# Kernel tuning notes

Hardware: AMD Instinct MI355X
Metric: run time of the kernel (lower is better)

Reference implementation:

```python
import jax, jax.numpy as jnp
import numpy as np

N, C, H, W = 4, 256, 64, 64
D = 128  # inter_channels = C // 2


def setup_inputs() -> dict:
    key = jax.random.key(0)
    ks = jax.random.split(key, 9)
    s = 0.05  # weight scale
    return {
        "x": jax.random.normal(ks[0], (N, C, H, W), jnp.float32),
        "Wg": jax.random.normal(ks[1], (D, C), jnp.float32) * s,
        "bg": jax.random.normal(ks[2], (D,), jnp.float32) * s,
        "Wt": jax.random.normal(ks[3], (D, C), jnp.float32) * s,
        "bt": jax.random.normal(ks[4], (D,), jnp.float32) * s,
        "Wp": jax.random.normal(ks[5], (D, C), jnp.float32) * s,
        "bp": jax.random.normal(ks[6], (D,), jnp.float32) * s,
        "Wz": jax.random.normal(ks[7], (C, D), jnp.float32) * s,
        "bz": jax.random.normal(ks[8], (C,), jnp.float32) * s,
    }


def reference(x, Wg, bg, Wt, bt, Wp, bp, Wz, bz):
    # NonLocalBlock, mode='embedded', dimension=2, bn_layer=False.
    # 1x1 convs are per-pixel linear maps over channels.
    n, c, h, w = x.shape
    xf = x.reshape(n, c, h * w)                                  # (N,C,S)
    g_x = jnp.einsum('dc,ncs->nds', Wg, xf) + bg[None, :, None]  # (N,D,S)
    th = jnp.einsum('dc,ncs->nds', Wt, xf) + bt[None, :, None]   # (N,D,S)
    ph = jnp.einsum('dc,ncs->nds', Wp, xf) + bp[None, :, None]   # (N,D,S)
    f = jnp.einsum('nds,ndt->nst', th, ph)                       # (N,S,S)
    att = jax.nn.softmax(f, axis=-1)
    y = jnp.einsum('nst,ndt->nds', att, g_x)                     # (N,D,S)
    w_y = jnp.einsum('cd,nds->ncs', Wz, y) + bz[None, :, None]   # (N,C,S)
    return (w_y + xf).reshape(n, c, h, w)
```

## Files before the change

### kernel.cpp

```cpp
#include <hip/hip_runtime.h>
#include <math.h>

#define N_ 4
#define C_ 256
#define D_ 128
#define S_ 4096
#define LOG2E 1.4426950408889634f
#define SPLIT 4
#define TPS 16

typedef __attribute__((ext_vector_type(4))) float f32x4;
typedef __attribute__((ext_vector_type(16))) float f32x16;
typedef __attribute__((ext_vector_type(8))) short short8;
typedef __attribute__((ext_vector_type(8))) unsigned short ushort8;
typedef __attribute__((ext_vector_type(4))) unsigned short ushort4v;

#define MFMA16(a, b, c) __builtin_amdgcn_mfma_f32_16x16x32_bf16((a), (b), (c), 0, 0, 0)
#define MFMA32(a, b, c) __builtin_amdgcn_mfma_f32_32x32x16_bf16((a), (b), (c), 0, 0, 0)

__device__ __forceinline__ unsigned short f2bf(float f) {
  union { float f; unsigned int u; } v; v.f = f;
  unsigned int r = v.u + 0x7fffu + ((v.u >> 16) & 1u);
  return (unsigned short)(r >> 16);
}
__device__ __forceinline__ float bf2f(unsigned short u) {
  union { unsigned int u; float f; } v; v.u = ((unsigned int)u) << 16;
  return v.f;
}
__device__ __forceinline__ unsigned cvtpk(float lo, float hi) {
  unsigned r;
  asm("v_cvt_pk_bf16_f32 %0, %1, %2" : "=v"(r) : "v"(lo), "v"(hi));
  return r;
}
__device__ __forceinline__ float vmax16(const f32x16& v) {
  float a = fmaxf(fmaxf(v[0], v[1]), fmaxf(v[2], v[3]));
  float b = fmaxf(fmaxf(v[4], v[5]), fmaxf(v[6], v[7]));
  float c = fmaxf(fmaxf(v[8], v[9]), fmaxf(v[10], v[11]));
  float d = fmaxf(fmaxf(v[12], v[13]), fmaxf(v[14], v[15]));
  return fmaxf(fmaxf(a, b), fmaxf(c, d));
}
__device__ __forceinline__ float vsum16(const f32x16& v) {
  float a = (v[0] + v[1]) + (v[2] + v[3]);
  float b = (v[4] + v[5]) + (v[6] + v[7]);
  float c = (v[8] + v[9]) + (v[10] + v[11]);
  float d = (v[12] + v[13]) + (v[14] + v[15]);
  return (a + b) + (c + d);
}
__device__ __forceinline__ void gload16(const void* g, void* l) {
  __builtin_amdgcn_global_load_lds((const __attribute__((address_space(1))) unsigned int*)g,
                                   (__attribute__((address_space(3))) unsigned int*)l,
                                   16, 0, 0);
}

__global__ void k_convw(const float* __restrict__ w0, const float* __restrict__ w1,
                        const float* __restrict__ w2, const float* __restrict__ w3,
                        unsigned short* __restrict__ d0, unsigned short* __restrict__ d1,
                        unsigned short* __restrict__ d2, unsigned short* __restrict__ d3) {
  int b = blockIdx.x;
  int w = b >> 4;
  int i = (b & 15) * 256 + threadIdx.x;
  const float* s = (w == 0) ? w0 : (w == 1) ? w1 : (w == 2) ? w2 : w3;
  unsigned short* d = (w == 0) ? d0 : (w == 1) ? d1 : (w == 2) ? d2 : d3;
  const float4* sp = reinterpret_cast<const float4*>(s) + (size_t)i * 2;
  float4 a = sp[0], c = sp[1];
  ushort8 o;
  o[0] = f2bf(a.x); o[1] = f2bf(a.y); o[2] = f2bf(a.z); o[3] = f2bf(a.w);
  o[4] = f2bf(c.x); o[5] = f2bf(c.y); o[6] = f2bf(c.z); o[7] = f2bf(c.w);
  reinterpret_cast<ushort8*>(d)[i] = o;
}

__global__ __launch_bounds__(256, 2) void k_proj(
    const float* __restrict__ x,
    const unsigned short* __restrict__ wg, const unsigned short* __restrict__ wt,
    const unsigned short* __restrict__ wp,
    const float* __restrict__ bg, const float* __restrict__ bt, const float* __restrict__ bp,
    unsigned short* __restrict__ qb, unsigned short* __restrict__ kb, unsigned short* __restrict__ vb)
{
  __shared__ __align__(16) unsigned short xs[C_ * 64];
  const int tid = threadIdx.x;
  const int n = blockIdx.x >> 6;
  const int s0 = (blockIdx.x & 63) << 6;
  const float* xsrc = x + (size_t)n * C_ * S_ + s0;
#pragma unroll
  for (int i = 0; i < 16; ++i) {
    int ch = i * 256 + tid;
    int c = ch >> 4, s4 = (ch & 15) << 2;
    float4 v = *reinterpret_cast<const float4*>(xsrc + (size_t)c * S_ + s4);
    ushort4v o;
    o[0] = f2bf(v.x); o[1] = f2bf(v.y); o[2] = f2bf(v.z); o[3] = f2bf(v.w);
    *reinterpret_cast<ushort4v*>(xs + c * 64 + s4) = o;
  }
  __syncthreads();
  const int lane = tid & 63, wid = tid >> 6;
  const int l15 = lane & 15, g = lane >> 4;
  const int scol = wid * 16 + l15;

  short8 bx[8];
#pragma unroll
  for (int kc = 0; kc < 8; ++kc) {
    int cb = kc * 32 + g * 8;
    short8 t;
#pragma unroll
    for (int j = 0; j < 8; ++j) t[j] = (short)xs[(cb + j) * 64 + scol];
    bx[kc] = t;
  }

  const f32x4 fz = {0.f, 0.f, 0.f, 0.f};
  for (int p = 0; p < 3; ++p) {
    const unsigned short* W = (p == 0) ? wg : ((p == 1) ? wt : wp);
    const float* bias = (p == 0) ? bg : ((p == 1) ? bt : bp);
    f32x4 acc[8];
#pragma unroll
    for (int dt = 0; dt < 8; ++dt) acc[dt] = fz;
#pragma unroll
    for (int dt = 0; dt < 8; ++dt) {
      const unsigned short* wrow = W + (size_t)(dt * 16 + l15) * C_ + g * 8;
#pragma unroll
      for (int kc = 0; kc < 8; ++kc) {
        short8 a = *reinterpret_cast<const short8*>(wrow + kc * 32);
        acc[dt] = MFMA16(a, bx[kc], acc[dt]);
      }
    }
    if (p == 0) {
#pragma unroll
      for (int dt = 0; dt < 8; ++dt) {
#pragma unroll
        for (int r = 0; r < 4; ++r) {
          int d = dt * 16 + 4 * g + r;
          vb[((size_t)n * D_ + d) * S_ + s0 + scol] = f2bf(acc[dt][r] + bias[d]);
        }
      }
    } else {
      unsigned short* dst = (p == 1) ? qb : kb;
      unsigned short* row = dst + ((size_t)(n * S_) + s0 + scol) * D_;
#pragma unroll
      for (int dt = 0; dt < 8; ++dt) {
        ushort4v o;
#pragma unroll
        for (int r = 0; r < 4; ++r) o[r] = f2bf(acc[dt][r] + bias[dt * 16 + 4 * g + r]);
        *reinterpret_cast<ushort4v*>(row + dt * 16 + 4 * g) = o;
      }
    }
  }
}

__global__ __launch_bounds__(256, 2) void k_attn(
    const unsigned short* __restrict__ qb, const unsigned short* __restrict__ kb,
    const unsigned short* __restrict__ vb,
    unsigned short* __restrict__ opart, float2* __restrict__ ml)
{
  __shared__ __align__(16) unsigned short ksm[2][64 * 128];
  __shared__ __align__(16) unsigned short vsm[2][128 * 64];
  const int tid = threadIdx.x, lane = tid & 63, w = tid >> 6;
  const int l31 = lane & 31, hi = lane >> 5;
  const int b = blockIdx.x;
  const int sp = b & 3, qt = (b >> 2) & 31, n = b >> 7;
  const int q0 = qt << 7;

  unsigned koff[4], voff[4], ubo[4];
#pragma unroll
  for (int j = 0; j < 4; ++j) {
    int f = j * 256 + tid;
    int kr = f >> 4, kc = f & 15;
    koff[j] = kr * D_ + ((kc ^ (kr & 7)) << 3);
    int vr = f >> 3, vc = f & 7;
    voff[j] = vr * S_ + ((vc ^ (vr & 7)) << 3);
    ubo[j] = (unsigned)(j * 256 + (tid & 192)) * 8;
  }
  const unsigned short* kb0 = kb + ((size_t)n * S_ + (size_t)sp * TPS * 64) * D_;
  const unsigned short* vb0 = vb + (size_t)n * D_ * S_ + sp * TPS * 64;

  auto stage = [&](int buf, int t) {
    const unsigned short* kt = kb0 + (size_t)t * 64 * D_;
    const unsigned short* vt = vb0 + t * 64;
#pragma unroll
    for (int j = 0; j < 4; ++j) gload16(kt + koff[j], &ksm[buf][ubo[j]]);
#pragma unroll
    for (int j = 0; j < 4; ++j) gload16(vt + voff[j], &vsm[buf][ubo[j]]);
  };

  stage(0, 0);

  const unsigned short* qsrc = qb + ((size_t)(n * S_) + q0 + w * 32 + l31) * D_;
  short8 qf[8];
#pragma unroll
  for (int k = 0; k < 8; ++k)
    qf[k] = *reinterpret_cast<const short8*>(qsrc + k * 16 + hi * 8);

  const f32x16 z16 = {0.f,0.f,0.f,0.f,0.f,0.f,0.f,0.f,0.f,0.f,0.f,0.f,0.f,0.f,0.f,0.f};
  f32x16 oacc[4];
#pragma unroll
  for (int db = 0; db < 4; ++db) oacc[db] = z16;
  float m_ = -3.4e38f, l_ = 0.f;

  __syncthreads();
  int cur = 0;

  for (int t = 0; t < TPS; ++t) {
    if (t + 1 < TPS) stage(cur ^ 1, t + 1);

    const unsigned short* ksb = ksm[cur];
    const unsigned short* vsb = vsm[cur];

    f32x16 pA = z16, pB = z16;
    __builtin_amdgcn_s_setprio(1);
#pragma unroll
    for (int ks = 0; ks < 8; ++ks) {
      int c = ks * 2 + hi;
      int r0 = l31, r1 = 32 + l31;
      short8 k0 = *reinterpret_cast<const short8*>(ksb + r0 * 128 + ((c ^ (r0 & 7)) << 3));
      short8 k1 = *reinterpret_cast<const short8*>(ksb + r1 * 128 + ((c ^ (r1 & 7)) << 3));
      pA = MFMA32(k0, qf[ks], pA);
      pB = MFMA32(k1, qf[ks], pB);
    }
    __builtin_amdgcn_s_setprio(0);

    float mrow = fmaxf(vmax16(pA), vmax16(pB));
    mrow = fmaxf(mrow, __shfl_xor(mrow, 32));
    if (!__all(mrow - m_ <= 8.0f)) {
      float mn = fmaxf(m_, mrow);
      float ss = exp2f((m_ - mn) * LOG2E);
      m_ = mn; l_ *= ss;
#pragma unroll
      for (int reg = 0; reg < 16; ++reg) {
        int rr = (reg & 3) + 8 * (reg >> 2) + 4 * hi;
        float sb = __shfl(ss, rr);
#pragma unroll
        for (int db = 0; db < 4; ++db) oacc[db][reg] *= sb;
      }
    }
#pragma unroll
    for (int i = 0; i < 16; ++i) pA[i] = exp2f((pA[i] - m_) * LOG2E);
#pragma unroll
    for (int i = 0; i < 16; ++i) pB[i] = exp2f((pB[i] - m_) * LOG2E);
    float rs = vsum16(pA) + vsum16(pB);
    l_ += rs + __shfl_xor(rs, 32);

    short8 pa[4];
#pragma unroll
    for (int ks = 0; ks < 4; ++ks) {
      const f32x16& p = (ks < 2) ? pA : pB;
      int ba = (ks & 1) * 8;
      unsigned ua0 = cvtpk(p[ba + 0], p[ba + 1]);
      unsigned ua1 = cvtpk(p[ba + 2], p[ba + 3]);
      unsigned ub0 = cvtpk(p[ba + 4], p[ba + 5]);
      unsigned ub1 = cvtpk(p[ba + 6], p[ba + 7]);
      unsigned x0 = (unsigned)__shfl_xor((int)(hi ? ua0 : ub0), 32);
      unsigned x1 = (unsigned)__shfl_xor((int)(hi ? ua1 : ub1), 32);
      union { unsigned u[4]; short8 s; } m;
      m.u[0] = hi ? x0 : ua0;  m.u[1] = hi ? x1 : ua1;
      m.u[2] = hi ? ub0 : x0;  m.u[3] = hi ? ub1 : x1;
      pa[ks] = m.s;
    }

    __builtin_amdgcn_s_setprio(1);
#pragma unroll
    for (int ks = 0; ks < 4; ++ks) {
      int c = ks * 2 + hi;
#pragma unroll
      for (int db = 0; db < 4; ++db) {
        int r = db * 32 + l31;
        short8 v = *reinterpret_cast<const short8*>(vsb + r * 64 + ((c ^ (r & 7)) << 3));
        oacc[db] = MFMA32(pa[ks], v, oacc[db]);
      }
    }
    __builtin_amdgcn_s_setprio(0);

    __syncthreads();
    cur ^= 1;
  }

  float linv = 1.f / l_;
  unsigned short* ob = opart + (((size_t)(n * SPLIT + sp)) * S_ + q0 + w * 32) * D_;
#pragma unroll
  for (int reg = 0; reg < 16; ++reg) {
    int rr = (reg & 3) + 8 * (reg >> 2) + 4 * hi;
    float li = __shfl(linv, rr);
#pragma unroll
    for (int db = 0; db < 4; ++db)
      ob[(size_t)rr * D_ + db * 32 + l31] = f2bf(oacc[db][reg] * li);
  }
  if (hi == 0) {
    ml[((size_t)(n * SPLIT + sp)) * S_ + q0 + w * 32 + l31] = make_float2(m_, l_);
  }
}

__global__ __launch_bounds__(256, 2) void k_final(
    const unsigned short* __restrict__ opart, const float2* __restrict__ ml,
    const unsigned short* __restrict__ wz, const float* __restrict__ bz,
    const float* __restrict__ x, float* __restrict__ out)
{
  __shared__ __align__(16) unsigned short ysm[32 * 128];
  __shared__ float wsm[32][4];
  const int tid = threadIdx.x, lane = tid & 63, wid = tid >> 6;
  const int l15 = lane & 15, g = lane >> 4;
  const int n = blockIdx.x >> 7, s0 = (blockIdx.x & 127) << 5;

  if (tid < 32) {
    int row = s0 + tid;
    float m0, l0, m1, l1, m2, l2, m3, l3;
    { float2 v = ml[(size_t)(n * 4 + 0) * S_ + row]; m0 = v.x; l0 = v.y; }
    { float2 v = ml[(size_t)(n * 4 + 1) * S_ + row]; m1 = v.x; l1 = v.y; }
    { float2 v = ml[(size_t)(n * 4 + 2) * S_ + row]; m2 = v.x; l2 = v.y; }
    { float2 v = ml[(size_t)(n * 4 + 3) * S_ + row]; m3 = v.x; l3 = v.y; }
    float M = fmaxf(fmaxf(m0, m1), fmaxf(m2, m3));
    float w0 = l0 * exp2f((m0 - M) * LOG2E);
    float w1 = l1 * exp2f((m1 - M) * LOG2E);
    float w2 = l2 * exp2f((m2 - M) * LOG2E);
    float w3 = l3 * exp2f((m3 - M) * LOG2E);
    float L = 1.f / (w0 + w1 + w2 + w3);
    wsm[tid][0] = w0 * L; wsm[tid][1] = w1 * L;
    wsm[tid][2] = w2 * L; wsm[tid][3] = w3 * L;
  }
  __syncthreads();

#pragma unroll
  for (int i = 0; i < 2; ++i) {
    int ch = i * 256 + tid;
    int row = ch >> 4, d8 = ch & 15;
    const unsigned short* p = opart + ((size_t)(n * 4) * S_ + s0 + row) * D_ + d8 * 8;
    ushort8 a0 = *reinterpret_cast<const ushort8*>(p);
    ushort8 a1 = *reinterpret_cast<const ushort8*>(p + (size_t)S_ * D_);
    ushort8 a2 = *reinterpret_cast<const ushort8*>(p + (size_t)2 * S_ * D_);
    ushort8 a3 = *reinterpret_cast<const ushort8*>(p + (size_t)3 * S_ * D_);
    float w0 = wsm[row][0], w1 = wsm[row][1], w2 = wsm[row][2], w3 = wsm[row][3];
    ushort8 o;
#pragma unroll
    for (int e = 0; e < 8; ++e) {
      float acc = bf2f(a0[e]) * w0 + bf2f(a1[e]) * w1 + bf2f(a2[e]) * w2 + bf2f(a3[e]) * w3;
      o[e] = f2bf(acc);
    }
    *reinterpret_cast<ushort8*>(ysm + row * 128 + ((d8 ^ (row & 7)) << 3)) = o;
  }
  __syncthreads();

  const int c0 = wid * 64;
  const f32x4 fz = {0.f, 0.f, 0.f, 0.f};
  f32x4 acc[4][2];
#pragma unroll
  for (int ct = 0; ct < 4; ++ct)
#pragma unroll
    for (int st = 0; st < 2; ++st) acc[ct][st] = fz;
#pragma unroll
  for (int kc = 0; kc < 4; ++kc) {
    short8 by[2];
#pragma unroll
    for (int st = 0; st < 2; ++st) {
      int r = st * 16 + l15;
      int ch = (kc * 4 + g) ^ (r & 7);
      by[st] = *reinterpret_cast<const short8*>(ysm + r * 128 + ch * 8);
    }
#pragma unroll
    for (int ct = 0; ct < 4; ++ct) {
      const short8 aw = *reinterpret_cast<const short8*>(
          wz + (size_t)(c0 + ct * 16 + l15) * D_ + kc * 32 + g * 8);
#pragma unroll
      for (int st = 0; st < 2; ++st) acc[ct][st] = MFMA16(aw, by[st], acc[ct][st]);
    }
  }
#pragma unroll
  for (int ct = 0; ct < 4; ++ct)
#pragma unroll
    for (int r = 0; r < 4; ++r) {
      int c = c0 + ct * 16 + 4 * g + r;
      float bias = bz[c];
#pragma unroll
      for (int st = 0; st < 2; ++st) {
        int s = s0 + st * 16 + l15;
        size_t idx = ((size_t)(n * C_ + c)) * S_ + s;
        out[idx] = acc[ct][st][r] + bias + x[idx];
      }
    }
}

extern "C" void kernel_launch(void* const* d_in, const int* in_sizes, int n_in,
                              void* d_out, int out_size, void* d_ws, size_t ws_size,
                              hipStream_t stream) {
  const float* x  = (const float*)d_in[0];
  const float* Wg = (const float*)d_in[1];
  const float* bg = (const float*)d_in[2];
  const float* Wt = (const float*)d_in[3];
  const float* bt = (const float*)d_in[4];
  const float* Wp = (const float*)d_in[5];
  const float* bp = (const float*)d_in[6];
  const float* Wz = (const float*)d_in[7];
  const float* bz = (const float*)d_in[8];
  float* out = (float*)d_out;
  char* ws = (char*)d_ws;
  const size_t MB = 1u << 20;
  unsigned short* qb    = (unsigned short*)(ws);
  unsigned short* kb    = (unsigned short*)(ws + 4 * MB);
  unsigned short* vb    = (unsigned short*)(ws + 8 * MB);
  unsigned short* opart = (unsigned short*)(ws + 12 * MB);
  float2*        mlbuf  = (float2*)(ws + 28 * MB);
  unsigned short* wgb   = (unsigned short*)(ws + 28 * MB + 524288);
  unsigned short* wtb   = (unsigned short*)(ws + 28 * MB + 524288 + 65536);
  unsigned short* wpb   = (unsigned short*)(ws + 28 * MB + 524288 + 131072);
  unsigned short* wzb   = (unsigned short*)(ws + 28 * MB + 524288 + 196608);

  k_convw<<<64, 256, 0, stream>>>(Wg, Wt, Wp, Wz, wgb, wtb, wpb, wzb);
  k_proj <<<256, 256, 0, stream>>>(x, wgb, wtb, wpb, bg, bt, bp, qb, kb, vb);
  k_attn <<<512, 256, 0, stream>>>(qb, kb, vb, opart, mlbuf);
  k_final<<<512, 256, 0, stream>>>(opart, mlbuf, wzb, bz, x, out);
}
```

Before: 113.6 us.

## Halve KV tile to 32 and split keys eight ways when workspace allows

Shrinks the attention KV tile from 64 to 32 keys, which halves LDS use per block and raises launch bounds to 4 blocks per CU. It also templates the split count, using 8 key slices (1024 blocks) when the workspace is large enough and falling back to 4 otherwise, with the merge kernel generalized to match. The goal is more occupancy and more blocks to fill the CUs. The cost is more loop iterations with a barrier each, a larger partial-output buffer, and more merge traffic in the final kernel.

New measurement: 172.2 us. +51.5%, slower.

```diff
diff --git a/kernel.cpp b/kernel.cpp
--- a/kernel.cpp
+++ b/kernel.cpp
@@ -6,8 +6,7 @@
 #define D_ 128
 #define S_ 4096
 #define LOG2E 1.4426950408889634f
-#define SPLIT 4
-#define TPS 16
+#define KVB 32
 
 typedef __attribute__((ext_vector_type(4))) float f32x4;
 typedef __attribute__((ext_vector_type(16))) float f32x16;
@@ -144,39 +143,42 @@
   }
 }
 
-__global__ __launch_bounds__(256, 2) void k_attn(
+template <int SP, int SPB>
+__global__ __launch_bounds__(256, 4) void k_attn(
     const unsigned short* __restrict__ qb, const unsigned short* __restrict__ kb,
     const unsigned short* __restrict__ vb,
     unsigned short* __restrict__ opart, float2* __restrict__ ml)
 {
-  __shared__ __align__(16) unsigned short ksm[2][64 * 128];
-  __shared__ __align__(16) unsigned short vsm[2][128 * 64];
+  constexpr int SLICE = S_ / SP;
+  constexpr int TPS = SLICE / KVB;
+  __shared__ __align__(16) unsigned short ksm[2][KVB * 128];
+  __shared__ __align__(16) unsigned short vsm[2][128 * KVB];
   const int tid = threadIdx.x, lane = tid & 63, w = tid >> 6;
   const int l31 = lane & 31, hi = lane >> 5;
   const int b = blockIdx.x;
-  const int sp = b & 3, qt = (b >> 2) & 31, n = b >> 7;
+  const int sp = b & (SP - 1), qt = (b >> SPB) & 31, n = b >> (5 + SPB);
   const int q0 = qt << 7;
 
-  unsigned koff[4], voff[4], ubo[4];
-#pragma unroll
-  for (int j = 0; j < 4; ++j) {
+  unsigned koff[2], voff[2], ubo[2];
+#pragma unroll
+  for (int j = 0; j < 2; ++j) {
     int f = j * 256 + tid;
     int kr = f >> 4, kc = f & 15;
     koff[j] = kr * D_ + ((kc ^ (kr & 7)) << 3);
-    int vr = f >> 3, vc = f & 7;
-    voff[j] = vr * S_ + ((vc ^ (vr & 7)) << 3);
+    int vr = f >> 2, vc = f & 3;
+    voff[j] = vr * S_ + ((vc ^ (vr & 3)) << 3);
     ubo[j] = (unsigned)(j * 256 + (tid & 192)) * 8;
   }
-  const unsigned short* kb0 = kb + ((size_t)n * S_ + (size_t)sp * TPS * 64) * D_;
-  const unsigned short* vb0 = vb + (size_t)n * D_ * S_ + sp * TPS * 64;
+  const unsigned short* kb0 = kb + ((size_t)n * S_ + sp * SLICE) * D_;
+  const unsigned short* vb0 = vb + (size_t)n * D_ * S_ + sp * SLICE;
 
   auto stage = [&](int buf, int t) {
-    const unsigned short* kt = kb0 + (size_t)t * 64 * D_;
-    const unsigned short* vt = vb0 + t * 64;
-#pragma unroll
-    for (int j = 0; j < 4; ++j) gload16(kt + koff[j], &ksm[buf][ubo[j]]);
-#pragma unroll
-    for (int j = 0; j < 4; ++j) gload16(vt + voff[j], &vsm[buf][ubo[j]]);
+    const unsigned short* kt = kb0 + (size_t)t * KVB * D_;
+    const unsigned short* vt = vb0 + t * KVB;
+#pragma unroll
+    for (int j = 0; j < 2; ++j) gload16(kt + koff[j], &ksm[buf][ubo[j]]);
+#pragma unroll
+    for (int j = 0; j < 2; ++j) gload16(vt + voff[j], &vsm[buf][ubo[j]]);
   };
 
   stage(0, 0);
@@ -202,20 +204,18 @@
     const unsigned short* ksb = ksm[cur];
     const unsigned short* vsb = vsm[cur];
 
-    f32x16 pA = z16, pB = z16;
+    f32x16 pA = z16;
     __builtin_amdgcn_s_setprio(1);
 #pragma unroll
     for (int ks = 0; ks < 8; ++ks) {
       int c = ks * 2 + hi;
-      int r0 = l31, r1 = 32 + l31;
+      int r0 = l31;
       short8 k0 = *reinterpret_cast<const short8*>(ksb + r0 * 128 + ((c ^ (r0 & 7)) << 3));
-      short8 k1 = *reinterpret_cast<const short8*>(ksb + r1 * 128 + ((c ^ (r1 & 7)) << 3));
       pA = MFMA32(k0, qf[ks], pA);
-      pB = MFMA32(k1, qf[ks], pB);
     }
     __builtin_amdgcn_s_setprio(0);
 
-    float mrow = fmaxf(vmax16(pA), vmax16(pB));
+    float mrow = vmax16(pA);
     mrow = fmaxf(mrow, __shfl_xor(mrow, 32));
     if (!__all(mrow - m_ <= 8.0f)) {
       float mn = fmaxf(m_, mrow);
@@ -231,36 +231,33 @@
     }
 #pragma unroll
     for (int i = 0; i < 16; ++i) pA[i] = exp2f((pA[i] - m_) * LOG2E);
-#pragma unroll
-    for (int i = 0; i < 16; ++i) pB[i] = exp2f((pB[i] - m_) * LOG2E);
-    float rs = vsum16(pA) + vsum16(pB);
+    float rs = vsum16(pA);
     l_ += rs + __shfl_xor(rs, 32);
 
-    short8 pa[4];
-#pragma unroll
-    for (int ks = 0; ks < 4; ++ks) {
-      const f32x16& p = (ks < 2) ? pA : pB;
-      int ba = (ks & 1) * 8;
-      unsigned ua0 = cvtpk(p[ba + 0], p[ba + 1]);
-      unsigned ua1 = cvtpk(p[ba + 2], p[ba + 3]);
-      unsigned ub0 = cvtpk(p[ba + 4], p[ba + 5]);
-      unsigned ub1 = cvtpk(p[ba + 6], p[ba + 7]);
+    short8 pa[2];
+#pragma unroll
+    for (int ks = 0; ks < 2; ++ks) {
+      int ba = ks * 8;
+      unsigned ua0 = cvtpk(pA[ba + 0], pA[ba + 1]);
+      unsigned ua1 = cvtpk(pA[ba + 2], pA[ba + 3]);
+      unsigned ub0 = cvtpk(pA[ba + 4], pA[ba + 5]);
+      unsigned ub1 = cvtpk(pA[ba + 6], pA[ba + 7]);
       unsigned x0 = (unsigned)__shfl_xor((int)(hi ? ua0 : ub0), 32);
       unsigned x1 = (unsigned)__shfl_xor((int)(hi ? ua1 : ub1), 32);
-      union { unsigned u[4]; short8 s; } m;
-      m.u[0] = hi ? x0 : ua0;  m.u[1] = hi ? x1 : ua1;
-      m.u[2] = hi ? ub0 : x0;  m.u[3] = hi ? ub1 : x1;
-      pa[ks] = m.s;
+      union { unsigned u[4]; short8 s; } mm;
+      mm.u[0] = hi ? x0 : ua0;  mm.u[1] = hi ? x1 : ua1;
+      mm.u[2] = hi ? ub0 : x0;  mm.u[3] = hi ? ub1 : x1;
+      pa[ks] = mm.s;
     }
 
     __builtin_amdgcn_s_setprio(1);
 #pragma unroll
-    for (int ks = 0; ks < 4; ++ks) {
+    for (int ks = 0; ks < 2; ++ks) {
       int c = ks * 2 + hi;
 #pragma unroll
       for (int db = 0; db < 4; ++db) {
         int r = db * 32 + l31;
-        short8 v = *reinterpret_cast<const short8*>(vsb + r * 64 + ((c ^ (r & 7)) << 3));
+        short8 v = *reinterpret_cast<const short8*>(vsb + r * KVB + ((c ^ (r & 3)) << 3));
         oacc[db] = MFMA32(pa[ks], v, oacc[db]);
       }
     }
@@ -271,7 +268,7 @@
   }
 
   float linv = 1.f / l_;
-  unsigned short* ob = opart + (((size_t)(n * SPLIT + sp)) * S_ + q0 + w * 32) * D_;
+  unsigned short* ob = opart + (((size_t)(n * SP + sp)) * S_ + q0 + w * 32) * D_;
 #pragma unroll
   for (int reg = 0; reg < 16; ++reg) {
     int rr = (reg & 3) + 8 * (reg >> 2) + 4 * hi;
@@ -281,36 +278,38 @@
       ob[(size_t)rr * D_ + db * 32 + l31] = f2bf(oacc[db][reg] * li);
   }
   if (hi == 0) {
-    ml[((size_t)(n * SPLIT + sp)) * S_ + q0 + w * 32 + l31] = make_float2(m_, l_);
-  }
-}
-
+    ml[((size_t)(n * SP + sp)) * S_ + q0 + w * 32 + l31] = make_float2(m_, l_);
+  }
+}
+
+template <int NP>
 __global__ __launch_bounds__(256, 2) void k_final(
     const unsigned short* __restrict__ opart, const float2* __restrict__ ml,
     const unsigned short* __restrict__ wz, const float* __restrict__ bz,
     const float* __restrict__ x, float* __restrict__ out)
 {
   __shared__ __align__(16) unsigned short ysm[32 * 128];
-  __shared__ float wsm[32][4];
+  __shared__ float wsm[32][NP];
   const int tid = threadIdx.x, lane = tid & 63, wid = tid >> 6;
   const int l15 = lane & 15, g = lane >> 4;
   const int n = blockIdx.x >> 7, s0 = (blockIdx.x & 127) << 5;
 
   if (tid < 32) {
     int row = s0 + tid;
-    float m0, l0, m1, l1, m2, l2, m3, l3;
-    { float2 v = ml[(size_t)(n * 4 + 0) * S_ + row]; m0 = v.x; l0 = v.y; }
-    { float2 v = ml[(size_t)(n * 4 + 1) * S_ + row]; m1 = v.x; l1 = v.y; }
-    { float2 v = ml[(size_t)(n * 4 + 2) * S_ + row]; m2 = v.x; l2 = v.y; }
-    { float2 v = ml[(size_t)(n * 4 + 3) * S_ + row]; m3 = v.x; l3 = v.y; }
-    float M = fmaxf(fmaxf(m0, m1), fmaxf(m2, m3));
-    float w0 = l0 * exp2f((m0 - M) * LOG2E);
-    float w1 = l1 * exp2f((m1 - M) * LOG2E);
-    float w2 = l2 * exp2f((m2 - M) * LOG2E);
-    float w3 = l3 * exp2f((m3 - M) * LOG2E);
-    float L = 1.f / (w0 + w1 + w2 + w3);
-    wsm[tid][0] = w0 * L; wsm[tid][1] = w1 * L;
-    wsm[tid][2] = w2 * L; wsm[tid][3] = w3 * L;
+    float mv[NP], lv[NP];
+    float M = -3.4e38f;
+#pragma unroll
+    for (int i = 0; i < NP; ++i) {
+      float2 v = ml[(size_t)(n * NP + i) * S_ + row];
+      mv[i] = v.x; lv[i] = v.y;
+      M = fmaxf(M, mv[i]);
+    }
+    float wsum = 0.f, wv[NP];
+#pragma unroll
+    for (int i = 0; i < NP; ++i) { wv[i] = lv[i] * exp2f((mv[i] - M) * LOG2E); wsum += wv[i]; }
+    float L = 1.f / wsum;
+#pragma unroll
+    for (int i = 0; i < NP; ++i) wsm[tid][i] = wv[i] * L;
   }
   __syncthreads();
 
@@ -318,18 +317,18 @@
   for (int i = 0; i < 2; ++i) {
     int ch = i * 256 + tid;
     int row = ch >> 4, d8 = ch & 15;
-    const unsigned short* p = opart + ((size_t)(n * 4) * S_ + s0 + row) * D_ + d8 * 8;
-    ushort8 a0 = *reinterpret_cast<const ushort8*>(p);
-    ushort8 a1 = *reinterpret_cast<const ushort8*>(p + (size_t)S_ * D_);
-    ushort8 a2 = *reinterpret_cast<const ushort8*>(p + (size_t)2 * S_ * D_);
-    ushort8 a3 = *reinterpret_cast<const ushort8*>(p + (size_t)3 * S_ * D_);
-    float w0 = wsm[row][0], w1 = wsm[row][1], w2 = wsm[row][2], w3 = wsm[row][3];
+    const unsigned short* p = opart + ((size_t)(n * NP) * S_ + s0 + row) * D_ + d8 * 8;
+    float acc[8] = {0.f, 0.f, 0.f, 0.f, 0.f, 0.f, 0.f, 0.f};
+#pragma unroll
+    for (int j = 0; j < NP; ++j) {
+      ushort8 a = *reinterpret_cast<const ushort8*>(p + (size_t)j * S_ * D_);
+      float wj = wsm[row][j];
+#pragma unroll
+      for (int e = 0; e < 8; ++e) acc[e] += bf2f(a[e]) * wj;
+    }
     ushort8 o;
 #pragma unroll
-    for (int e = 0; e < 8; ++e) {
-      float acc = bf2f(a0[e]) * w0 + bf2f(a1[e]) * w1 + bf2f(a2[e]) * w2 + bf2f(a3[e]) * w3;
-      o[e] = f2bf(acc);
-    }
+    for (int e = 0; e < 8; ++e) o[e] = f2bf(acc[e]);
     *reinterpret_cast<ushort8*>(ysm + row * 128 + ((d8 ^ (row & 7)) << 3)) = o;
   }
   __syncthreads();
@@ -388,18 +387,26 @@
   float* out = (float*)d_out;
   char* ws = (char*)d_ws;
   const size_t MB = 1u << 20;
+  const bool big = ws_size >= 46 * MB;
+
   unsigned short* qb    = (unsigned short*)(ws);
   unsigned short* kb    = (unsigned short*)(ws + 4 * MB);
   unsigned short* vb    = (unsigned short*)(ws + 8 * MB);
   unsigned short* opart = (unsigned short*)(ws + 12 * MB);
-  float2*        mlbuf  = (float2*)(ws + 28 * MB);
-  unsigned short* wgb   = (unsigned short*)(ws + 28 * MB + 524288);
-  unsigned short* wtb   = (unsigned short*)(ws + 28 * MB + 524288 + 65536);
-  unsigned short* wpb   = (unsigned short*)(ws + 28 * MB + 524288 + 131072);
-  unsigned short* wzb   = (unsigned short*)(ws + 28 * MB + 524288 + 196608);
+  size_t mloff = big ? 44 * MB : 28 * MB;
+  float2*        mlbuf  = (float2*)(ws + mloff);
+  unsigned short* wgb   = (unsigned short*)(ws + mloff + 1 * MB);
+  unsigned short* wtb   = (unsigned short*)(ws + mloff + 1 * MB + 65536);
+  unsigned short* wpb   = (unsigned short*)(ws + mloff + 1 * MB + 131072);
+  unsigned short* wzb   = (unsigned short*)(ws + mloff + 1 * MB + 196608);
 
   k_convw<<<64, 256, 0, stream>>>(Wg, Wt, Wp, Wz, wgb, wtb, wpb, wzb);
   k_proj <<<256, 256, 0, stream>>>(x, wgb, wtb, wpb, bg, bt, bp, qb, kb, vb);
-  k_attn <<<512, 256, 0, stream>>>(qb, kb, vb, opart, mlbuf);
-  k_final<<<512, 256, 0, stream>>>(opart, mlbuf, wzb, bz, x, out);
-}
+  if (big) {
+    k_attn<8, 3><<<1024, 256, 0, stream>>>(qb, kb, vb, opart, mlbuf);
+    k_final<8> <<<512, 256, 0, stream>>>(opart, mlbuf, wzb, bz, x, out);
+  } else {
+    k_attn<4, 2><<<512, 256, 0, stream>>>(qb, kb, vb, opart, mlbuf);
+    k_final<4> <<<512, 256, 0, stream>>>(opart, mlbuf, wzb, bz, x, out);
+  }
+}
```

## Split projection blocks per output and use 512-thread attention blocks sharing K/V tiles

Applied to the files above, without the earlier changes.

k_proj now launches one block per (projection, batch, spatial tile), 768 blocks instead of 256. Each block computes a single projection, which adds parallelism but reloads and converts the x tile three times. k_attn now uses 512-thread blocks covering 256 query rows, so each staged K/V tile is shared by 8 waves instead of 4, halving K/V traffic per query at the cost of fewer, larger blocks (256). The k_final changes are cosmetic loop restructuring.

After: 105.3 us. 7.3% less time.

```diff
diff --git a/kernel.cpp b/kernel.cpp
--- a/kernel.cpp
+++ b/kernel.cpp
@@ -69,7 +69,7 @@
   reinterpret_cast<ushort8*>(d)[i] = o;
 }
 
-__global__ __launch_bounds__(256, 2) void k_proj(
+__global__ __launch_bounds__(256, 3) void k_proj(
     const float* __restrict__ x,
     const unsigned short* __restrict__ wg, const unsigned short* __restrict__ wt,
     const unsigned short* __restrict__ wp,
@@ -78,7 +78,8 @@
 {
   __shared__ __align__(16) unsigned short xs[C_ * 64];
   const int tid = threadIdx.x;
-  const int n = blockIdx.x >> 6;
+  const int p = blockIdx.x >> 8;
+  const int n = (blockIdx.x >> 6) & 3;
   const int s0 = (blockIdx.x & 63) << 6;
   const float* xsrc = x + (size_t)n * C_ * S_ + s0;
 #pragma unroll
@@ -105,46 +106,44 @@
     bx[kc] = t;
   }
 
+  const unsigned short* W = (p == 0) ? wg : ((p == 1) ? wt : wp);
+  const float* bias = (p == 0) ? bg : ((p == 1) ? bt : bp);
   const f32x4 fz = {0.f, 0.f, 0.f, 0.f};
-  for (int p = 0; p < 3; ++p) {
-    const unsigned short* W = (p == 0) ? wg : ((p == 1) ? wt : wp);
-    const float* bias = (p == 0) ? bg : ((p == 1) ? bt : bp);
-    f32x4 acc[8];
-#pragma unroll
-    for (int dt = 0; dt < 8; ++dt) acc[dt] = fz;
+  f32x4 acc[8];
+#pragma unroll
+  for (int dt = 0; dt < 8; ++dt) acc[dt] = fz;
+#pragma unroll
+  for (int dt = 0; dt < 8; ++dt) {
+    const unsigned short* wrow = W + (size_t)(dt * 16 + l15) * C_ + g * 8;
+#pragma unroll
+    for (int kc = 0; kc < 8; ++kc) {
+      short8 a = *reinterpret_cast<const short8*>(wrow + kc * 32);
+      acc[dt] = MFMA16(a, bx[kc], acc[dt]);
+    }
+  }
+  if (p == 0) {
 #pragma unroll
     for (int dt = 0; dt < 8; ++dt) {
-      const unsigned short* wrow = W + (size_t)(dt * 16 + l15) * C_ + g * 8;
-#pragma unroll
-      for (int kc = 0; kc < 8; ++kc) {
-        short8 a = *reinterpret_cast<const short8*>(wrow + kc * 32);
-        acc[dt] = MFMA16(a, bx[kc], acc[dt]);
+#pragma unroll
+      for (int r = 0; r < 4; ++r) {
+        int d = dt * 16 + 4 * g + r;
+        vb[((size_t)n * D_ + d) * S_ + s0 + scol] = f2bf(acc[dt][r] + bias[d]);
       }
     }
-    if (p == 0) {
-#pragma unroll
-      for (int dt = 0; dt < 8; ++dt) {
-#pragma unroll
-        for (int r = 0; r < 4; ++r) {
-          int d = dt * 16 + 4 * g + r;
-          vb[((size_t)n * D_ + d) * S_ + s0 + scol] = f2bf(acc[dt][r] + bias[d]);
-        }
-      }
-    } else {
-      unsigned short* dst = (p == 1) ? qb : kb;
-      unsigned short* row = dst + ((size_t)(n * S_) + s0 + scol) * D_;
-#pragma unroll
-      for (int dt = 0; dt < 8; ++dt) {
-        ushort4v o;
-#pragma unroll
-        for (int r = 0; r < 4; ++r) o[r] = f2bf(acc[dt][r] + bias[dt * 16 + 4 * g + r]);
-        *reinterpret_cast<ushort4v*>(row + dt * 16 + 4 * g) = o;
-      }
-    }
-  }
-}
-
-__global__ __launch_bounds__(256, 2) void k_attn(
+  } else {
+    unsigned short* dst = (p == 1) ? qb : kb;
+    unsigned short* row = dst + ((size_t)(n * S_) + s0 + scol) * D_;
+#pragma unroll
+    for (int dt = 0; dt < 8; ++dt) {
+      ushort4v o;
+#pragma unroll
+      for (int r = 0; r < 4; ++r) o[r] = f2bf(acc[dt][r] + bias[dt * 16 + 4 * g + r]);
+      *reinterpret_cast<ushort4v*>(row + dt * 16 + 4 * g) = o;
+    }
+  }
+}
+
+__global__ __launch_bounds__(512, 2) void k_attn(
     const unsigned short* __restrict__ qb, const unsigned short* __restrict__ kb,
     const unsigned short* __restrict__ vb,
     unsigned short* __restrict__ opart, float2* __restrict__ ml)
@@ -154,18 +153,18 @@
   const int tid = threadIdx.x, lane = tid & 63, w = tid >> 6;
   const int l31 = lane & 31, hi = lane >> 5;
   const int b = blockIdx.x;
-  const int sp = b & 3, qt = (b >> 2) & 31, n = b >> 7;
-  const int q0 = qt << 7;
-
-  unsigned koff[4], voff[4], ubo[4];
-#pragma unroll
-  for (int j = 0; j < 4; ++j) {
-    int f = j * 256 + tid;
+  const int sp = b & 3, qt = (b >> 2) & 15, n = b >> 6;
+  const int q0 = qt << 8;
+
+  unsigned koff[2], voff[2], ubo[2];
+#pragma unroll
+  for (int j = 0; j < 2; ++j) {
+    int f = j * 512 + tid;
     int kr = f >> 4, kc = f & 15;
     koff[j] = kr * D_ + ((kc ^ (kr & 7)) << 3);
     int vr = f >> 3, vc = f & 7;
     voff[j] = vr * S_ + ((vc ^ (vr & 7)) << 3);
-    ubo[j] = (unsigned)(j * 256 + (tid & 192)) * 8;
+    ubo[j] = (unsigned)(j * 512 + (tid & 448)) * 8;
   }
   const unsigned short* kb0 = kb + ((size_t)n * S_ + (size_t)sp * TPS * 64) * D_;
   const unsigned short* vb0 = vb + (size_t)n * D_ * S_ + sp * TPS * 64;
@@ -174,9 +173,9 @@
     const unsigned short* kt = kb0 + (size_t)t * 64 * D_;
     const unsigned short* vt = vb0 + t * 64;
 #pragma unroll
-    for (int j = 0; j < 4; ++j) gload16(kt + koff[j], &ksm[buf][ubo[j]]);
-#pragma unroll
-    for (int j = 0; j < 4; ++j) gload16(vt + voff[j], &vsm[buf][ubo[j]]);
+    for (int j = 0; j < 2; ++j) gload16(kt + koff[j], &ksm[buf][ubo[j]]);
+#pragma unroll
+    for (int j = 0; j < 2; ++j) gload16(vt + voff[j], &vsm[buf][ubo[j]]);
   };
 
   stage(0, 0);
@@ -247,10 +246,10 @@
       unsigned ub1 = cvtpk(p[ba + 6], p[ba + 7]);
       unsigned x0 = (unsigned)__shfl_xor((int)(hi ? ua0 : ub0), 32);
       unsigned x1 = (unsigned)__shfl_xor((int)(hi ? ua1 : ub1), 32);
-      union { unsigned u[4]; short8 s; } m;
-      m.u[0] = hi ? x0 : ua0;  m.u[1] = hi ? x1 : ua1;
-      m.u[2] = hi ? ub0 : x0;  m.u[3] = hi ? ub1 : x1;
-      pa[ks] = m.s;
+      union { unsigned u[4]; short8 s; } mm;
+      mm.u[0] = hi ? x0 : ua0;  mm.u[1] = hi ? x1 : ua1;
+      mm.u[2] = hi ? ub0 : x0;  mm.u[3] = hi ? ub1 : x1;
+      pa[ks] = mm.s;
     }
 
     __builtin_amdgcn_s_setprio(1);
@@ -298,19 +297,20 @@
 
   if (tid < 32) {
     int row = s0 + tid;
-    float m0, l0, m1, l1, m2, l2, m3, l3;
-    { float2 v = ml[(size_t)(n * 4 + 0) * S_ + row]; m0 = v.x; l0 = v.y; }
-    { float2 v = ml[(size_t)(n * 4 + 1) * S_ + row]; m1 = v.x; l1 = v.y; }
-    { float2 v = ml[(size_t)(n * 4 + 2) * S_ + row]; m2 = v.x; l2 = v.y; }
-    { float2 v = ml[(size_t)(n * 4 + 3) * S_ + row]; m3 = v.x; l3 = v.y; }
-    float M = fmaxf(fmaxf(m0, m1), fmaxf(m2, m3));
-    float w0 = l0 * exp2f((m0 - M) * LOG2E);
-    float w1 = l1 * exp2f((m1 - M) * LOG2E);
-    float w2 = l2 * exp2f((m2 - M) * LOG2E);
-    float w3 = l3 * exp2f((m3 - M) * LOG2E);
-    float L = 1.f / (w0 + w1 + w2 + w3);
-    wsm[tid][0] = w0 * L; wsm[tid][1] = w1 * L;
-    wsm[tid][2] = w2 * L; wsm[tid][3] = w3 * L;
+    float mv[4], lv[4];
+    float M = -3.4e38f;
+#pragma unroll
+    for (int i = 0; i < 4; ++i) {
+      float2 v = ml[(size_t)(n * 4 + i) * S_ + row];
+      mv[i] = v.x; lv[i] = v.y;
+      M = fmaxf(M, mv[i]);
+    }
+    float wsum = 0.f, wv[4];
+#pragma unroll
+    for (int i = 0; i < 4; ++i) { wv[i] = lv[i] * exp2f((mv[i] - M) * LOG2E); wsum += wv[i]; }
+    float L = 1.f / wsum;
+#pragma unroll
+    for (int i = 0; i < 4; ++i) wsm[tid][i] = wv[i] * L;
   }
   __syncthreads();
 
@@ -319,17 +319,17 @@
     int ch = i * 256 + tid;
     int row = ch >> 4, d8 = ch & 15;
     const unsigned short* p = opart + ((size_t)(n * 4) * S_ + s0 + row) * D_ + d8 * 8;
-    ushort8 a0 = *reinterpret_cast<const ushort8*>(p);
-    ushort8 a1 = *reinterpret_cast<const ushort8*>(p + (size_t)S_ * D_);
-    ushort8 a2 = *reinterpret_cast<const ushort8*>(p + (size_t)2 * S_ * D_);
-    ushort8 a3 = *reinterpret_cast<const ushort8*>(p + (size_t)3 * S_ * D_);
-    float w0 = wsm[row][0], w1 = wsm[row][1], w2 = wsm[row][2], w3 = wsm[row][3];
+    float acc[8] = {0.f, 0.f, 0.f, 0.f, 0.f, 0.f, 0.f, 0.f};
+#pragma unroll
+    for (int j = 0; j < 4; ++j) {
+      ushort8 a = *reinterpret_cast<const ushort8*>(p + (size_t)j * S_ * D_);
+      float wj = wsm[row][j];
+#pragma unroll
+      for (int e = 0; e < 8; ++e) acc[e] += bf2f(a[e]) * wj;
+    }
     ushort8 o;
 #pragma unroll
-    for (int e = 0; e < 8; ++e) {
-      float acc = bf2f(a0[e]) * w0 + bf2f(a1[e]) * w1 + bf2f(a2[e]) * w2 + bf2f(a3[e]) * w3;
-      o[e] = f2bf(acc);
-    }
+    for (int e = 0; e < 8; ++e) o[e] = f2bf(acc[e]);
     *reinterpret_cast<ushort8*>(ysm + row * 128 + ((d8 ^ (row & 7)) << 3)) = o;
   }
   __syncthreads();
@@ -399,7 +399,7 @@
   unsigned short* wzb   = (unsigned short*)(ws + 28 * MB + 524288 + 196608);
 
   k_convw<<<64, 256, 0, stream>>>(Wg, Wt, Wp, Wz, wgb, wtb, wpb, wzb);
-  k_proj <<<256, 256, 0, stream>>>(x, wgb, wtb, wpb, bg, bt, bp, qb, kb, vb);
-  k_attn <<<512, 256, 0, stream>>>(qb, kb, vb, opart, mlbuf);
+  k_proj <<<768, 256, 0, stream>>>(x, wgb, wtb, wpb, bg, bt, bp, qb, kb, vb);
+  k_attn <<<256, 512, 0, stream>>>(qb, kb, vb, opart, mlbuf);
   k_final<<<512, 256, 0, stream>>>(opart, mlbuf, wzb, bz, x, out);
 }
```
